# Optimization experiments

Measured on AMD Instinct MI355X. Metric: run time of the kernel, lower is better.

Reference implementation:

```python
import jax, jax.numpy as jnp
import numpy as np

B, LMAX, T_OUT, VOCAB, EMB, CVEC, HID, OUT = 8192, 12, 10, 36, 300, 256, 256, 512


def setup_inputs() -> dict:
    key = jax.random.key(0)
    ks = jax.random.split(key, 16)
    s = lambda fan: 1.0 / np.sqrt(fan)
    u = lambda k, shape, b: jax.random.uniform(k, shape, jnp.float32, -b, b)
    inp = {
        'words': jax.random.randint(ks[0], (B, LMAX), 0, VOCAB),
        'lengths': 1 + jax.random.randint(ks[1], (B,), 0, LMAX),  # in [1, LMAX]
        'emb_table': jax.random.normal(ks[2], (VOCAB, EMB), jnp.float32),
        'enc_w': u(ks[3], (CVEC, EMB), s(EMB)),
        'enc_b': u(ks[4], (CVEC,), s(EMB)),
        'wih_f': u(ks[5], (4 * HID, CVEC), s(HID)),
        'whh_f': u(ks[6], (4 * HID, HID), s(HID)),
        'bih_f': u(ks[7], (4 * HID,), s(HID)),
        'bhh_f': u(ks[8], (4 * HID,), s(HID)),
        'wih_b': u(ks[9], (4 * HID, CVEC), s(HID)),
        'whh_b': u(ks[10], (4 * HID, HID), s(HID)),
        'bih_b': u(ks[11], (4 * HID,), s(HID)),
        'bhh_b': u(ks[12], (4 * HID,), s(HID)),
        'out_w': u(ks[13], (OUT, 2 * HID), s(2 * HID)),
        'out_b': u(ks[14], (OUT,), s(2 * HID)),
    }
    return inp


def _interp_words(emb_table, words, lengths):
    # bilinear resize (L,300)->(10,300) with align_corners=True; width unchanged
    # so it is exact linear interpolation along the char axis.
    def one(word_row, L):
        Lf = (L - 1).astype(jnp.float32)
        pos = jnp.arange(T_OUT, dtype=jnp.float32) * Lf / (T_OUT - 1)  # (10,)
        i0 = jnp.floor(pos).astype(jnp.int32)
        i1 = jnp.minimum(i0 + 1, L - 1).astype(jnp.int32)
        f = (pos - i0.astype(jnp.float32))[:, None]
        e = emb_table[word_row]  # (LMAX, EMB)
        return e[i0] * (1.0 - f) + e[i1] * f  # (10, EMB)
    return jax.vmap(one)(words, lengths)  # (B, 10, EMB)


def _lstm(seq, wih, whh, bih, bhh):
    # seq: (T, B, In); PyTorch gate order i, f, g, o
    bsz = seq.shape[1]
    h0 = jnp.zeros((bsz, HID), seq.dtype)
    c0 = jnp.zeros((bsz, HID), seq.dtype)

    def step(carry, x_t):
        h, c = carry
        g = x_t @ wih.T + h @ whh.T + (bih + bhh)
        i, f, gg, o = jnp.split(g, 4, axis=-1)
        c = jax.nn.sigmoid(f) * c + jax.nn.sigmoid(i) * jnp.tanh(gg)
        h = jax.nn.sigmoid(o) * jnp.tanh(c)
        return (h, c), h

    _, hs = jax.lax.scan(step, (h0, c0), seq)
    return hs  # (T, B, HID)


def reference(words, lengths, emb_table, enc_w, enc_b, wih_f, whh_f, bih_f, bhh_f,
              wih_b, whh_b, bih_b, bhh_b, out_w, out_b):
    emb = _interp_words(emb_table, words, lengths)              # (B, 10, 300)
    cv = jax.nn.relu(emb @ enc_w.T + enc_b)                     # (B, 10, 256)
    seq = jnp.transpose(cv, (1, 0, 2))                          # (10, B, 256)
    h_f = _lstm(seq, wih_f, whh_f, bih_f, bhh_f)                # (10, B, 256)
    h_b = _lstm(seq[::-1], wih_b, whh_b, bih_b, bhh_b)[::-1]    # (10, B, 256)
    rec = jnp.concatenate([h_f, h_b], axis=-1)                  # (10, B, 512)
    out = rec @ out_w.T + out_b                                 # (10, B, 512)
    return jnp.transpose(out, (1, 0, 2))                        # (B, 10, 512)
```

## Files before the change

kernel.cpp:

```cpp
#include <hip/hip_runtime.h>
#include <hip/hip_fp16.h>

typedef _Float16 f16;
typedef _Float16 f16x2 __attribute__((ext_vector_type(2)));
typedef _Float16 f16x8 __attribute__((ext_vector_type(8)));
typedef float    f32x4 __attribute__((ext_vector_type(4)));

#define NB   8192
#define TOUT 10
#define LMAX 12
#define EMB  300

__device__ __forceinline__ float sigm_(float x) {
    return __builtin_amdgcn_rcpf(1.0f + __builtin_amdgcn_exp2f(x * -1.44269504f));
}
__device__ __forceinline__ float tanh_(float x) {
    return 1.0f - 2.0f * __builtin_amdgcn_rcpf(1.0f + __builtin_amdgcn_exp2f(x * 2.88539008f));
}
__device__ __forceinline__ f16x2 pk_f16(float a, float b) {
    return __builtin_bit_cast(f16x2, __builtin_amdgcn_cvt_pkrtz(a, b));
}

__global__ __launch_bounds__(256) void pack_w2(
    const float* __restrict__ wih_f, const float* __restrict__ whh_f,
    const float* __restrict__ wih_b, const float* __restrict__ whh_b,
    f16* __restrict__ Wp) {
    int idx = blockIdx.x * 256 + threadIdx.x;
    int d   = idx >> 19;
    int r   = idx & 524287;
    int tile = r >> 9;
    int e    = r & 511;
    int kc = tile >> 6, nt = tile & 63;
    int khi = e >> 7, rem = e & 127, nl = rem >> 3, klo = rem & 7;
    int n = nt * 16 + nl;
    int k = kc * 32 + khi * 8 + klo;
    int gate = (n >> 4) & 3;
    int u = ((n >> 6) << 4) | (n & 15);
    int srow = gate * 256 + u;
    const float* wih = d ? wih_b : wih_f;
    const float* whh = d ? whh_b : whh_f;
    float v = (k < 256) ? wih[srow * 256 + k] : whh[srow * 256 + (k - 256)];
    Wp[idx] = (f16)v;
}

__global__ __launch_bounds__(256) void pack_bias(
    const float* __restrict__ bih_f, const float* __restrict__ bhh_f,
    const float* __restrict__ bih_b, const float* __restrict__ bhh_b,
    float* __restrict__ bp) {
    int idx = blockIdx.x * 256 + threadIdx.x;
    int d = idx >> 10, n = idx & 1023;
    int gate = (n >> 4) & 3;
    int u = ((n >> 6) << 4) | (n & 15);
    int srow = gate * 256 + u;
    bp[idx] = d ? (bih_b[srow] + bhh_b[srow]) : (bih_f[srow] + bhh_f[srow]);
}

__global__ __launch_bounds__(256) void pack_w3(
    const float* __restrict__ out_w, f16* __restrict__ W3p) {
    int idx = blockIdx.x * 256 + threadIdx.x;
    int tile = idx >> 9, e = idx & 511;
    int kc = tile >> 5, nt = tile & 31;
    int khi = e >> 7, rem = e & 127, nl = rem >> 3, klo = rem & 7;
    int n = nt * 16 + nl, k = kc * 32 + khi * 8 + klo;
    W3p[idx] = (f16)out_w[n * 512 + k];
}

__global__ __launch_bounds__(256) void enc_proj(
    const float* __restrict__ tab, const float* __restrict__ ew,
    const float* __restrict__ eb, float* __restrict__ P) {
    int v = blockIdx.x, j = threadIdx.x;
    const float* a = tab + v * EMB;
    const float* w = ew + j * EMB;
    float s = 0.0f;
    for (int k = 0; k < EMB; ++k) s += a[k] * w[k];
    P[v * 256 + j] = s + eb[j];
}

__global__ __launch_bounds__(256) void build_seq(
    const int* __restrict__ words, const int* __restrict__ lengths,
    const float* __restrict__ P, f16* __restrict__ seqp) {
    int gi = blockIdx.x * 256 + threadIdx.x;
    int bl  = gi & 15;
    int khi = (gi >> 4) & 3;
    int kc  = (gi >> 6) & 7;
    int mt  = (gi >> 9) & 511;
    int t   = gi >> 18;
    int b = mt * 16 + bl;
    int L = lengths[b];
    float pos = ((float)t * (float)(L - 1)) / 9.0f;
    int i0 = (int)pos;
    float f = pos - (float)i0;
    int i1 = min(i0 + 1, L - 1);
    int c0 = words[b * LMAX + i0];
    int c1 = words[b * LMAX + i1];
    const float* p0 = P + c0 * 256 + kc * 32 + khi * 8;
    const float* p1 = P + c1 * 256 + kc * 32 + khi * 8;
    f16x8 r;
#pragma unroll
    for (int j = 0; j < 8; ++j) {
        float v = p0[j] * (1.0f - f) + p1[j] * f;
        v = fmaxf(v, 0.0f);
        r[j] = (f16)v;
    }
    *((f16x8*)seqp + gi) = r;
}

__global__ __launch_bounds__(1024) void lstm_fused(
    const f16* __restrict__ seqp, const f16* __restrict__ Wp,
    const float* __restrict__ bp, f16* __restrict__ hcat) {
    const int dir  = blockIdx.x >> 7;
    const int r0t  = (blockIdx.x & 127) << 2;
    const int wave = threadIdx.x >> 6;
    const int lane = threadIdx.x & 63;
    const int l16  = lane & 15;
    const int quad = lane >> 4;

    __shared__ __align__(16) f16 hbuf[2][4 * 8 * 512];

    {
        f16x8 z = {(f16)0, (f16)0, (f16)0, (f16)0, (f16)0, (f16)0, (f16)0, (f16)0};
        for (int i = threadIdx.x; i < 2048; i += 1024) ((f16x8*)hbuf[0])[i] = z;
    }

    const float* bpd = bp + dir * 1024 + wave * 64;
    float bias_l[4];
#pragma unroll
    for (int nt = 0; nt < 4; ++nt) bias_l[nt] = bpd[nt * 16 + l16];

    const f16* Wd = Wp + dir * 524288 + (wave * 4) * 512 + lane * 8;

    const int slot = wave >> 1;
    const int ofs0 = (((wave & 1) * 2 + (l16 >> 3)) * 16 + quad * 4) * 8 + (l16 & 7);
    const int tile_lo = (r0t * 16 + dir * 8 + slot) * 512;

    float cst[4][4];
#pragma unroll
    for (int m = 0; m < 4; ++m)
#pragma unroll
        for (int q = 0; q < 4; ++q) cst[m][q] = 0.0f;

    __syncthreads();

    int cur = 0;
#pragma unroll 1
    for (int step = 0; step < TOUT; ++step) {
        const int t = dir ? (9 - step) : step;
        const f16* hb_r = hbuf[cur] + lane * 8;
        f16*       hb_w = hbuf[cur ^ 1];

        f32x4 acc[4][4];
#pragma unroll
        for (int m = 0; m < 4; ++m)
#pragma unroll
            for (int nt = 0; nt < 4; ++nt)
#pragma unroll
                for (int q = 0; q < 4; ++q) acc[m][nt][q] = bias_l[nt];

        const f16* seqt = seqp + (size_t)(t * 512 + r0t) * 4096 + lane * 8;

#pragma unroll 1
        for (int kc = 0; kc < 8; ++kc) {
            f16x8 bfrag[4];
#pragma unroll
            for (int nt = 0; nt < 4; ++nt)
                bfrag[nt] = *(const f16x8*)(Wd + (kc * 64 + nt) * 512);
            f16x8 afrag[4];
#pragma unroll
            for (int m = 0; m < 4; ++m)
                afrag[m] = *(const f16x8*)(seqt + (m * 8 + kc) * 512);
#pragma unroll
            for (int m = 0; m < 4; ++m)
#pragma unroll
                for (int nt = 0; nt < 4; ++nt)
                    acc[m][nt] = __builtin_amdgcn_mfma_f32_16x16x32_f16(
                        afrag[m], bfrag[nt], acc[m][nt], 0, 0, 0);
        }
#pragma unroll 1
        for (int kcl = 0; kcl < 8; ++kcl) {
            int kc = kcl + 8;
            f16x8 bfrag[4];
#pragma unroll
            for (int nt = 0; nt < 4; ++nt)
                bfrag[nt] = *(const f16x8*)(Wd + (kc * 64 + nt) * 512);
            f16x8 afrag[4];
#pragma unroll
            for (int m = 0; m < 4; ++m)
                afrag[m] = *(const f16x8*)(hb_r + (m * 8 + kcl) * 512);
#pragma unroll
            for (int m = 0; m < 4; ++m)
#pragma unroll
                for (int nt = 0; nt < 4; ++nt)
                    acc[m][nt] = __builtin_amdgcn_mfma_f32_16x16x32_f16(
                        afrag[m], bfrag[nt], acc[m][nt], 0, 0, 0);
        }

        f16* hct = hcat + ((size_t)t * 4194304 + tile_lo);
#pragma unroll
        for (int m = 0; m < 4; ++m) {
#pragma unroll
            for (int q = 0; q < 4; ++q) {
                float iv = acc[m][0][q];
                float fv = acc[m][1][q];
                float gv = acc[m][2][q];
                float ov = acc[m][3][q];
                float c = sigm_(fv) * cst[m][q] + sigm_(iv) * tanh_(gv);
                cst[m][q] = c;
                f16 hv = (f16)(sigm_(ov) * tanh_(c));
                int wt = ofs0 + q * 8;
                hb_w[(m * 8 + slot) * 512 + wt] = hv;
                hct[m * 8192 + wt] = hv;
            }
        }

        __syncthreads();
        cur ^= 1;
    }
}

__global__ __launch_bounds__(512) void out_gemm(
    const f16* __restrict__ hcat, const f16* __restrict__ W3p,
    const float* __restrict__ out_b, float* __restrict__ out) {
    const int mt0  = blockIdx.x << 2;
    const int wave = threadIdx.x >> 6;
    const int lane = threadIdx.x & 63;
    const int l16  = lane & 15;
    const int quad = lane >> 4;
    const int n0   = wave * 64;

    float bias_l[4];
#pragma unroll
    for (int nt = 0; nt < 4; ++nt) bias_l[nt] = out_b[n0 + nt * 16 + l16];

    f32x4 acc[4][4];
#pragma unroll
    for (int m = 0; m < 4; ++m)
#pragma unroll
        for (int nt = 0; nt < 4; ++nt)
#pragma unroll
            for (int q = 0; q < 4; ++q) acc[m][nt][q] = bias_l[nt];

#pragma unroll 2
    for (int kc = 0; kc < 16; ++kc) {
        f16x8 a[4], b[4];
#pragma unroll
        for (int m = 0; m < 4; ++m)
            a[m] = *(const f16x8*)(hcat + ((size_t)((mt0 + m) * 16 + kc) * 512 + lane * 8));
#pragma unroll
        for (int nt = 0; nt < 4; ++nt)
            b[nt] = *(const f16x8*)(W3p + ((kc * 32 + wave * 4 + nt) * 512 + lane * 8));
#pragma unroll
        for (int m = 0; m < 4; ++m)
#pragma unroll
            for (int nt = 0; nt < 4; ++nt)
                acc[m][nt] = __builtin_amdgcn_mfma_f32_16x16x32_f16(a[m], b[nt], acc[m][nt], 0, 0, 0);
    }

#pragma unroll
    for (int m = 0; m < 4; ++m) {
#pragma unroll
        for (int nt = 0; nt < 4; ++nt) {
#pragma unroll
            for (int q = 0; q < 4; ++q) {
                int R = mt0 * 16 + m * 16 + quad * 4 + q;
                int t = R >> 13;
                int b = R & 8191;
                out[(size_t)(b * 10 + t) * 512 + n0 + nt * 16 + l16] = acc[m][nt][q];
            }
        }
    }
}

extern "C" void kernel_launch(void* const* d_in, const int* in_sizes, int n_in,
                              void* d_out, int out_size, void* d_ws, size_t ws_size,
                              hipStream_t stream) {
    const int*   words   = (const int*)d_in[0];
    const int*   lengths = (const int*)d_in[1];
    const float* tab     = (const float*)d_in[2];
    const float* enc_w   = (const float*)d_in[3];
    const float* enc_b   = (const float*)d_in[4];
    const float* wih_f   = (const float*)d_in[5];
    const float* whh_f   = (const float*)d_in[6];
    const float* bih_f   = (const float*)d_in[7];
    const float* bhh_f   = (const float*)d_in[8];
    const float* wih_b   = (const float*)d_in[9];
    const float* whh_b   = (const float*)d_in[10];
    const float* bih_b   = (const float*)d_in[11];
    const float* bhh_b   = (const float*)d_in[12];
    const float* out_w   = (const float*)d_in[13];
    const float* out_b   = (const float*)d_in[14];
    float* out = (float*)d_out;

    char* ws = (char*)d_ws;
    f16*   Wp   = (f16*)(ws + 0);
    f16*   W3p  = (f16*)(ws + 2097152);
    float* bp   = (float*)(ws + 2621440);
    float* P    = (float*)(ws + 2629632);
    f16*   seqp = (f16*)(ws + 2666496);
    f16*   hcat = (f16*)(ws + 44609536);

    pack_w2<<<4096, 256, 0, stream>>>(wih_f, whh_f, wih_b, whh_b, Wp);
    pack_bias<<<8, 256, 0, stream>>>(bih_f, bhh_f, bih_b, bhh_b, bp);
    pack_w3<<<1024, 256, 0, stream>>>(out_w, W3p);
    enc_proj<<<36, 256, 0, stream>>>(tab, enc_w, enc_b, P);
    build_seq<<<10240, 256, 0, stream>>>(words, lengths, P, seqp);
    lstm_fused<<<256, 1024, 0, stream>>>(seqp, Wp, bp, hcat);
    out_gemm<<<1280, 512, 0, stream>>>(hcat, W3p, out_b, out);
}
```

Before: 471.9 us.

## Prefetch next timestep's input sequence into LDS asynchronously and raise MFMA priority

```diff
diff --git a/kernel.cpp b/kernel.cpp
--- a/kernel.cpp
+++ b/kernel.cpp
@@ -19,6 +19,12 @@
 }
 __device__ __forceinline__ f16x2 pk_f16(float a, float b) {
     return __builtin_bit_cast(f16x2, __builtin_amdgcn_cvt_pkrtz(a, b));
+}
+
+__device__ __forceinline__ void gl_lds16(const f16* g, f16* l) {
+    __builtin_amdgcn_global_load_lds(
+        (const __attribute__((address_space(1))) void*)g,
+        (__attribute__((address_space(3))) void*)l, 16, 0, 0);
 }
 
 __global__ __launch_bounds__(256) void pack_w2(
@@ -115,19 +121,28 @@
     const int l16  = lane & 15;
     const int quad = lane >> 4;
 
-    __shared__ __align__(16) f16 hbuf[2][4 * 8 * 512];
+    __shared__ __align__(16) f16 hbuf[2][16384];
+    __shared__ __align__(16) f16 sbuf[2][16384];
 
     {
         f16x8 z = {(f16)0, (f16)0, (f16)0, (f16)0, (f16)0, (f16)0, (f16)0, (f16)0};
         for (int i = threadIdx.x; i < 2048; i += 1024) ((f16x8*)hbuf[0])[i] = z;
     }
 
+    {
+        const int t0 = dir ? 9 : 0;
+        const f16* s0 = seqp + (size_t)(t0 * 512 + r0t) * 4096;
+        gl_lds16(s0 + threadIdx.x * 8,        &sbuf[0][wave * 512]);
+        gl_lds16(s0 + 8192 + threadIdx.x * 8, &sbuf[0][8192 + wave * 512]);
+    }
+
     const float* bpd = bp + dir * 1024 + wave * 64;
     float bias_l[4];
 #pragma unroll
     for (int nt = 0; nt < 4; ++nt) bias_l[nt] = bpd[nt * 16 + l16];
 
-    const f16* Wd = Wp + dir * 524288 + (wave * 4) * 512 + lane * 8;
+    const f16* Wu = Wp + dir * 524288 + wave * 2048;
+    const int  wo = lane * 8;
 
     const int slot = wave >> 1;
     const int ofs0 = (((wave & 1) * 2 + (l16 >> 3)) * 16 + quad * 4) * 8 + (l16 & 7);
@@ -145,7 +160,16 @@
 #pragma unroll 1
     for (int step = 0; step < TOUT; ++step) {
         const int t = dir ? (9 - step) : step;
-        const f16* hb_r = hbuf[cur] + lane * 8;
+
+        if (step != 9) {
+            const int tn = dir ? (t - 1) : (t + 1);
+            const f16* ns = seqp + (size_t)(tn * 512 + r0t) * 4096;
+            gl_lds16(ns + threadIdx.x * 8,        &sbuf[cur ^ 1][wave * 512]);
+            gl_lds16(ns + 8192 + threadIdx.x * 8, &sbuf[cur ^ 1][8192 + wave * 512]);
+        }
+
+        const f16* sb   = &sbuf[cur][lane * 8];
+        const f16* hb_r = &hbuf[cur][lane * 8];
         f16*       hb_w = hbuf[cur ^ 1];
 
         f32x4 acc[4][4];
@@ -155,43 +179,46 @@
             for (int nt = 0; nt < 4; ++nt)
 #pragma unroll
                 for (int q = 0; q < 4; ++q) acc[m][nt][q] = bias_l[nt];
-
-        const f16* seqt = seqp + (size_t)(t * 512 + r0t) * 4096 + lane * 8;
 
 #pragma unroll 1
         for (int kc = 0; kc < 8; ++kc) {
+            const f16* wk = Wu + kc * 32768;
             f16x8 bfrag[4];
 #pragma unroll
             for (int nt = 0; nt < 4; ++nt)
-                bfrag[nt] = *(const f16x8*)(Wd + (kc * 64 + nt) * 512);
+                bfrag[nt] = *(const f16x8*)(wk + nt * 512 + wo);
             f16x8 afrag[4];
 #pragma unroll
             for (int m = 0; m < 4; ++m)
-                afrag[m] = *(const f16x8*)(seqt + (m * 8 + kc) * 512);
+                afrag[m] = *(const f16x8*)(sb + (m * 8 + kc) * 512);
+            __builtin_amdgcn_s_setprio(1);
 #pragma unroll
             for (int m = 0; m < 4; ++m)
 #pragma unroll
                 for (int nt = 0; nt < 4; ++nt)
                     acc[m][nt] = __builtin_amdgcn_mfma_f32_16x16x32_f16(
                         afrag[m], bfrag[nt], acc[m][nt], 0, 0, 0);
+            __builtin_amdgcn_s_setprio(0);
         }
 #pragma unroll 1
         for (int kcl = 0; kcl < 8; ++kcl) {
-            int kc = kcl + 8;
+            const f16* wk = Wu + (kcl + 8) * 32768;
             f16x8 bfrag[4];
 #pragma unroll
             for (int nt = 0; nt < 4; ++nt)
-                bfrag[nt] = *(const f16x8*)(Wd + (kc * 64 + nt) * 512);
+                bfrag[nt] = *(const f16x8*)(wk + nt * 512 + wo);
             f16x8 afrag[4];
 #pragma unroll
             for (int m = 0; m < 4; ++m)
                 afrag[m] = *(const f16x8*)(hb_r + (m * 8 + kcl) * 512);
+            __builtin_amdgcn_s_setprio(1);
 #pragma unroll
             for (int m = 0; m < 4; ++m)
 #pragma unroll
                 for (int nt = 0; nt < 4; ++nt)
                     acc[m][nt] = __builtin_amdgcn_mfma_f32_16x16x32_f16(
                         afrag[m], bfrag[nt], acc[m][nt], 0, 0, 0);
+            __builtin_amdgcn_s_setprio(0);
         }
 
         f16* hct = hcat + ((size_t)t * 4194304 + tile_lo);
```

Measured after the change: 456.4 us. 3.3% less time.
